# Kernel tuning notes

Hardware: AMD Instinct MI355X
Metric: run time of the kernel (lower is better)

## Reference

```python
import jax, jax.numpy as jnp
import numpy as np

N_EMB = 1024
N_HEADS = 16


def setup_inputs() -> dict:
    key = jax.random.key(0)
    k1, k2, k3 = jax.random.split(key, 3)
    x = jax.random.normal(k1, (2, 2048, N_EMB), dtype=jnp.float32)
    # qkv linear params (torch Linear: y = x @ W.T + b; store W as [in, 3*in])
    W_qkv = jax.random.normal(k2, (N_EMB, 3 * N_EMB), dtype=jnp.float32) * (1.0 / np.sqrt(N_EMB))
    b_qkv = jax.random.normal(k3, (3 * N_EMB,), dtype=jnp.float32) * 0.02
    return {"x": x, "W_qkv": W_qkv, "b_qkv": b_qkv}


def reference(x, W_qkv, b_qkv):
    B, S, D = x.shape
    H = N_HEADS
    Dh = D // H
    qkv = x @ W_qkv + b_qkv                       # [B, S, 3D]
    q, k, v = jnp.split(qkv, 3, axis=-1)
    # [B, S, D] -> [B, H, S, Dh]
    q = q.reshape(B, S, H, Dh).transpose(0, 2, 1, 3)
    k = k.reshape(B, S, H, Dh).transpose(0, 2, 1, 3)
    v = v.reshape(B, S, H, Dh).transpose(0, 2, 1, 3)
    scores = jnp.einsum("bhqd,bhkd->bhqk", q, k) * (1.0 / np.sqrt(Dh))
    attn = jax.nn.softmax(scores, axis=-1)        # no causal mask in original
    out = jnp.einsum("bhqk,bhkd->bhqd", attn, v)  # [B, H, S, Dh]
    return out.transpose(0, 2, 1, 3).reshape(B, S, D)
```

## Files before the change

kernel.cpp:

```cpp
#include <hip/hip_runtime.h>

#define S_LEN 2048
#define D_EMB 1024
#define H_CNT 16
#define DHD   64
#define N_QKV 3072

typedef __attribute__((ext_vector_type(8))) short short8;
typedef __attribute__((ext_vector_type(4))) float f32x4;
typedef unsigned short u16;

__device__ __forceinline__ u16 f2bf(float f) {
  unsigned u = __float_as_uint(f);
  u += 0x7FFFu + ((u >> 16) & 1u);
  return (u16)(u >> 16);
}

__device__ __forceinline__ unsigned cvtpk(float lo, float hi) {
  unsigned r;
  asm("v_cvt_pk_bf16_f32 %0, %1, %2" : "=v"(r) : "v"(lo), "v"(hi));
  return r;
}

__device__ __forceinline__ void gload16(const void* g, void* lds) {
  __builtin_amdgcn_global_load_lds(
      (const __attribute__((address_space(1))) void*)g,
      (__attribute__((address_space(3))) void*)lds, 16, 0, 0);
}

__global__ __launch_bounds__(256) void cvt_x_kern(const float* __restrict__ x,
                                                  u16* __restrict__ xb) {
  int i = blockIdx.x * 256 + threadIdx.x;
  float4 v = ((const float4*)x)[i];
  unsigned* o = (unsigned*)&((ushort4*)xb)[i];
  o[0] = cvtpk(v.x, v.y);
  o[1] = cvtpk(v.z, v.w);
}

__global__ __launch_bounds__(256) void cvt_wt_kern(const float* __restrict__ w,
                                                   u16* __restrict__ wt) {
  __shared__ u16 tile[64][65];
  const int ct = blockIdx.x, kt = blockIdx.y, t = threadIdx.x;
#pragma unroll
  for (int i = 0; i < 4; ++i) {
    int idx = t + i * 256;
    int kk = idx >> 4, c4 = (idx & 15) * 4;
    float4 v = *(const float4*)(w + (size_t)(kt * 64 + kk) * N_QKV + ct * 64 + c4);
    tile[kk][c4 + 0] = f2bf(v.x);
    tile[kk][c4 + 1] = f2bf(v.y);
    tile[kk][c4 + 2] = f2bf(v.z);
    tile[kk][c4 + 3] = f2bf(v.w);
  }
  __syncthreads();
#pragma unroll
  for (int i = 0; i < 2; ++i) {
    int id = t + i * 256;
    int c = id >> 3, k8 = (id & 7) * 8;
    short8 o;
#pragma unroll
    for (int j = 0; j < 8; ++j) o[j] = (short)tile[k8 + j][c];
    *(short8*)&wt[(size_t)(ct * 64 + c) * D_EMB + kt * 64 + k8] = o;
  }
}

__global__ __launch_bounds__(256) void qkv_gemm_kern(
    const u16* __restrict__ xb, const u16* __restrict__ wt,
    const float* __restrict__ bias,
    u16* __restrict__ qo, u16* __restrict__ ko, u16* __restrict__ vo) {
  __shared__ __align__(16) u16 SM[128 * 128];
  u16* As = SM;
  u16* Bs = SM + 128 * 64;
  const int t = threadIdx.x;
  const int w = t >> 6, l = t & 63, lr = l & 15, lg = l >> 4;
  const int wr = w >> 1, wc = w & 1;
  const int row0 = blockIdx.x * 128, col0 = blockIdx.y * 128;
  const int srow = l >> 3, scol = (l & 7) * 16;
  const int tsel = col0 >> 10;
  const bool ctq = (tsel < 2);

  f32x4 acc[4][4];
#pragma unroll
  for (int m = 0; m < 4; ++m)
#pragma unroll
    for (int n = 0; n < 4; ++n) acc[m][n] = (f32x4){0.f, 0.f, 0.f, 0.f};

  const int ldrow = w * 32;
  for (int ki = 0; ki < 16; ++ki) {
    int k0 = ki * 64;
#pragma unroll
    for (int c = 0; c < 4; ++c) {
      int tr = ldrow + c * 8 + srow;
      int sc = scol ^ ((tr & 7) << 4);
      gload16((const char*)xb + (size_t)(row0 + tr) * (D_EMB * 2) + k0 * 2 + sc,
              (char*)As + (ldrow + c * 8) * 128);
      gload16((const char*)wt + (size_t)(col0 + tr) * (D_EMB * 2) + k0 * 2 + sc,
              (char*)Bs + (ldrow + c * 8) * 128);
    }
    __syncthreads();
    const u16* Ab = ctq ? Bs : As;
    const u16* Bb = ctq ? As : Bs;
    const int ar0 = ctq ? wc * 64 : wr * 64;
    const int br0 = ctq ? wr * 64 : wc * 64;
    short8 bfr[4][2];
#pragma unroll
    for (int n = 0; n < 4; ++n) {
      int br = br0 + n * 16 + lr;
#pragma unroll
      for (int kk = 0; kk < 2; ++kk)
        bfr[n][kk] = *(const short8*)&Bb[(br << 6) + ((kk * 32 + lg * 8) ^ ((br & 7) << 3))];
    }
#pragma unroll
    for (int m = 0; m < 4; ++m) {
      int ar = ar0 + m * 16 + lr;
      short8 a0 = *(const short8*)&Ab[(ar << 6) + ((lg * 8) ^ ((ar & 7) << 3))];
      short8 a1 = *(const short8*)&Ab[(ar << 6) + ((32 + lg * 8) ^ ((ar & 7) << 3))];
#pragma unroll
      for (int n = 0; n < 4; ++n) {
        acc[m][n] = __builtin_amdgcn_mfma_f32_16x16x32_bf16(a0, bfr[n][0], acc[m][n], 0, 0, 0);
        acc[m][n] = __builtin_amdgcn_mfma_f32_16x16x32_bf16(a1, bfr[n][1], acc[m][n], 0, 0, 0);
      }
    }
    __syncthreads();
  }

  const int bb = row0 >> 11;
  if (ctq) {
    const float scl = (tsel == 0) ? (0.125f * 1.44269504f) : 1.0f;
    u16* dst = (tsel == 0) ? qo : ko;
#pragma unroll
    for (int m = 0; m < 4; ++m) {
      int qc0 = wc * 64 + m * 16 + lg * 4;
      float4 bn = *(const float4*)&bias[col0 + qc0];
#pragma unroll
      for (int n = 0; n < 4; ++n) {
        int s = wr * 64 + n * 16 + lr;
        uint2 pk;
        pk.x = cvtpk((acc[m][n][0] + bn.x) * scl, (acc[m][n][1] + bn.y) * scl);
        pk.y = cvtpk((acc[m][n][2] + bn.z) * scl, (acc[m][n][3] + bn.w) * scl);
        *(uint2*)&SM[(s << 7) + (qc0 ^ ((s & 7) << 3))] = pk;
      }
    }
    __syncthreads();
    const int c = t & 15, rl = t >> 4;
#pragma unroll
    for (int pass = 0; pass < 8; ++pass) {
      int s = pass * 16 + rl;
      short8 v = *(const short8*)&SM[(s << 7) + ((c ^ (s & 7)) << 3)];
      int d = (col0 + c * 8) & 1023, hh = d >> 6, dh = d & 63;
      *(short8*)(dst + ((size_t)(bb * H_CNT + hh) * S_LEN + (row0 & 2047) + s) * DHD + dh) = v;
    }
  } else {
#pragma unroll
    for (int n = 0; n < 4; ++n) {
      int qc = wc * 64 + n * 16 + lr;
      float bn = bias[col0 + qc];
#pragma unroll
      for (int m = 0; m < 4; ++m) {
        int s0l = wr * 64 + m * 16 + lg * 4;
        uint2 pk;
        pk.x = cvtpk(acc[m][n][0] + bn, acc[m][n][1] + bn);
        pk.y = cvtpk(acc[m][n][2] + bn, acc[m][n][3] + bn);
        *(uint2*)&SM[(qc << 7) + (s0l ^ ((qc & 7) << 3))] = pk;
      }
    }
    __syncthreads();
    const int c = t & 15, rl = t >> 4;
#pragma unroll
    for (int pass = 0; pass < 8; ++pass) {
      int qc = pass * 16 + rl;
      short8 v = *(const short8*)&SM[(qc << 7) + ((c ^ (qc & 7)) << 3)];
      int d = (col0 + qc) & 1023, hh = d >> 6, dh = d & 63;
      *(short8*)(vo + ((size_t)(bb * H_CNT + hh) * DHD + dh) * S_LEN +
                 (row0 & 2047) + c * 8) = v;
    }
  }
}

__global__ __launch_bounds__(256) void attn_kern(
    const u16* __restrict__ qp, const u16* __restrict__ kp,
    const u16* __restrict__ vtp, float* __restrict__ out) {
  __shared__ __align__(16) u16 Ks[2][64 * 64];
  __shared__ __align__(16) u16 Vs[2][64 * 64];
  __shared__ __align__(16) u16 Ps[4][16 * 64];
  const int t = threadIdx.x;
  const int w = t >> 6, l = t & 63, lr = l & 15, lg = l >> 4;
  const int qt = blockIdx.x, bh = blockIdx.y;
  const int b = bh >> 4, h = bh & 15;
  const int srow = l >> 3, scol = (l & 7) * 16;

  const u16* qbase = qp + ((size_t)bh * S_LEN + qt * 64 + w * 16) * DHD;
  short8 qf[2];
#pragma unroll
  for (int kk = 0; kk < 2; ++kk)
    qf[kk] = *(const short8*)(qbase + lr * DHD + kk * 32 + lg * 8);

  float mrun = -__builtin_inff(), lsum = 0.f;
  f32x4 oacc[4];
#pragma unroll
  for (int ct = 0; ct < 4; ++ct) oacc[ct] = (f32x4){0.f, 0.f, 0.f, 0.f};

  const char* kt_g = (const char*)(kp + (size_t)bh * S_LEN * DHD);
  const char* vt_g = (const char*)(vtp + (size_t)bh * DHD * S_LEN);

#define ATTN_STAGE(it, buf)                                                     \
  {                                                                             \
    int kv0 = (it) * 64;                                                        \
    _Pragma("unroll") for (int c = 0; c < 2; ++c) {                             \
      int r8 = w * 16 + c * 8;                                                  \
      int row = r8 + srow;                                                      \
      int sc = scol ^ ((row & 7) << 4);                                         \
      gload16(kt_g + (size_t)(kv0 + row) * 128 + sc, (char*)Ks[buf] + r8 * 128);\
      gload16(vt_g + (size_t)row * (S_LEN * 2) + kv0 * 2 + sc,                  \
              (char*)Vs[buf] + r8 * 128);                                       \
    }                                                                           \
  }

  ATTN_STAGE(0, 0)
  __syncthreads();

  for (int it = 0; it < S_LEN / 64; ++it) {
    int cur = it & 1;
    if (it < S_LEN / 64 - 1) ATTN_STAGE(it + 1, cur ^ 1)

    f32x4 st[4];
#pragma unroll
    for (int k2 = 0; k2 < 4; ++k2) st[k2] = (f32x4){0.f, 0.f, 0.f, 0.f};
#pragma unroll
    for (int kk = 0; kk < 2; ++kk)
#pragma unroll
      for (int k2 = 0; k2 < 4; ++k2) {
        int ar = k2 * 16 + lr;
        short8 a = *(const short8*)&Ks[cur][(ar << 6) +
                                           ((kk * 32 + lg * 8) ^ ((ar & 7) << 3))];
        st[k2] = __builtin_amdgcn_mfma_f32_16x16x32_bf16(a, qf[kk], st[k2], 0, 0, 0);
      }

    float mx = -__builtin_inff();
#pragma unroll
    for (int k2 = 0; k2 < 4; ++k2)
#pragma unroll
      for (int r = 0; r < 4; ++r) mx = fmaxf(mx, st[k2][r]);
    mx = fmaxf(mx, __shfl_xor(mx, 16, 64));
    mx = fmaxf(mx, __shfl_xor(mx, 32, 64));
    if (!__all(mx - mrun <= 8.0f)) {
      float mnew = fmaxf(mrun, mx);
      float fsc = exp2f(mrun - mnew);
      float fr[4];
#pragma unroll
      for (int r = 0; r < 4; ++r) fr[r] = __shfl(fsc, lg * 4 + r, 64);
#pragma unroll
      for (int ct = 0; ct < 4; ++ct)
#pragma unroll
        for (int r = 0; r < 4; ++r) oacc[ct][r] *= fr[r];
      lsum *= fsc;
      mrun = mnew;
    }
    float rs = 0.f;
#pragma unroll
    for (int k2 = 0; k2 < 4; ++k2) {
      float p0 = exp2f(st[k2][0] - mrun), p1 = exp2f(st[k2][1] - mrun);
      float p2 = exp2f(st[k2][2] - mrun), p3 = exp2f(st[k2][3] - mrun);
      rs += (p0 + p1) + (p2 + p3);
      int key0 = k2 * 16 + lg * 4;
      int e = key0 ^ ((lr & 7) << 3);
      *(unsigned*)&Ps[w][(lr << 6) + e + 0] = cvtpk(p0, p1);
      *(unsigned*)&Ps[w][(lr << 6) + e + 2] = cvtpk(p2, p3);
    }
    rs += __shfl_xor(rs, 16, 64);
    rs += __shfl_xor(rs, 32, 64);
    lsum += rs;

    short8 pa[2];
#pragma unroll
    for (int kk = 0; kk < 2; ++kk)
      pa[kk] = *(const short8*)&Ps[w][(lr << 6) + ((kk * 32 + lg * 8) ^ ((lr & 7) << 3))];
#pragma unroll
    for (int ct = 0; ct < 4; ++ct)
#pragma unroll
      for (int kk = 0; kk < 2; ++kk) {
        int br = ct * 16 + lr;
        short8 bv = *(const short8*)&Vs[cur][(br << 6) +
                                            ((kk * 32 + lg * 8) ^ ((br & 7) << 3))];
        oacc[ct] = __builtin_amdgcn_mfma_f32_16x16x32_bf16(pa[kk], bv, oacc[ct], 0, 0, 0);
      }
    __syncthreads();
  }

  float inv = 1.0f / lsum;
  float invr[4];
#pragma unroll
  for (int r = 0; r < 4; ++r) invr[r] = __shfl(inv, lg * 4 + r, 64);
  const int qg0 = qt * 64 + w * 16 + lg * 4;
#pragma unroll
  for (int ct = 0; ct < 4; ++ct) {
    int col = h * 64 + ct * 16 + lr;
#pragma unroll
    for (int r = 0; r < 4; ++r)
      out[((size_t)b * S_LEN + qg0 + r) * D_EMB + col] = oacc[ct][r] * invr[r];
  }
}

extern "C" void kernel_launch(void* const* d_in, const int* in_sizes, int n_in,
                              void* d_out, int out_size, void* d_ws, size_t ws_size,
                              hipStream_t stream) {
  (void)in_sizes; (void)n_in; (void)out_size; (void)ws_size;
  const float* x  = (const float*)d_in[0];
  const float* Wq = (const float*)d_in[1];
  const float* bq = (const float*)d_in[2];
  float* out = (float*)d_out;
  char* ws = (char*)d_ws;
  u16* xb = (u16*)(ws);
  u16* wt = (u16*)(ws + (size_t)8  * 1024 * 1024);
  u16* qb = (u16*)(ws + (size_t)14 * 1024 * 1024);
  u16* kb = (u16*)(ws + (size_t)22 * 1024 * 1024);
  u16* vb = (u16*)(ws + (size_t)30 * 1024 * 1024);

  cvt_x_kern <<<4096, 256, 0, stream>>>(x, xb);
  cvt_wt_kern<<<dim3(48, 16), 256, 0, stream>>>(Wq, wt);
  qkv_gemm_kern<<<dim3(32, 24), 256, 0, stream>>>(xb, wt, bq, qb, kb, vb);
  attn_kern  <<<dim3(32, 32), 256, 0, stream>>>(qb, kb, vb, out);
}
```

Measured before the change: 196.5 us.

## Keep P in registers by permuting K rows at load time, drop LDS P round-trip

The probability tile is no longer written to and re-read from shared memory. K rows are instead loaded into LDS in a permuted order (tau mapping), so the MFMA score output layout already matches the A-operand layout needed for the PV MFMA, and P is packed straight from registers into bf16. The KV loop is also unrolled by two with compile-time buffer indices and pointer-increment addressing. This removes LDS writes and reads plus the associated latency per tile, but relies on the permutation being correct for the key/value pairing, since the softmax sum is order-independent while V must use the same key order.

Result: faster. 190.4 us (-3.1%).

```diff
diff --git a/kernel.cpp b/kernel.cpp
--- a/kernel.cpp
+++ b/kernel.cpp
@@ -8,6 +8,7 @@
 
 typedef __attribute__((ext_vector_type(8))) short short8;
 typedef __attribute__((ext_vector_type(4))) float f32x4;
+typedef __attribute__((ext_vector_type(4))) unsigned u32x4;
 typedef unsigned short u16;
 
 __device__ __forceinline__ u16 f2bf(float f) {
@@ -181,7 +182,6 @@
     const u16* __restrict__ vtp, float* __restrict__ out) {
   __shared__ __align__(16) u16 Ks[2][64 * 64];
   __shared__ __align__(16) u16 Vs[2][64 * 64];
-  __shared__ __align__(16) u16 Ps[4][16 * 64];
   const int t = threadIdx.x;
   const int w = t >> 6, l = t & 63, lr = l & 15, lg = l >> 4;
   const int qt = blockIdx.x, bh = blockIdx.y;
@@ -199,91 +199,92 @@
 #pragma unroll
   for (int ct = 0; ct < 4; ++ct) oacc[ct] = (f32x4){0.f, 0.f, 0.f, 0.f};
 
-  const char* kt_g = (const char*)(kp + (size_t)bh * S_LEN * DHD);
-  const char* vt_g = (const char*)(vtp + (size_t)bh * DHD * S_LEN);
-
-#define ATTN_STAGE(it, buf)                                                     \
-  {                                                                             \
-    int kv0 = (it) * 64;                                                        \
-    _Pragma("unroll") for (int c = 0; c < 2; ++c) {                             \
-      int r8 = w * 16 + c * 8;                                                  \
-      int row = r8 + srow;                                                      \
-      int sc = scol ^ ((row & 7) << 4);                                         \
-      gload16(kt_g + (size_t)(kv0 + row) * 128 + sc, (char*)Ks[buf] + r8 * 128);\
-      gload16(vt_g + (size_t)row * (S_LEN * 2) + kv0 * 2 + sc,                  \
-              (char*)Vs[buf] + r8 * 128);                                       \
-    }                                                                           \
-  }
-
-  ATTN_STAGE(0, 0)
+  int koff[2], voff[2];
+#pragma unroll
+  for (int c = 0; c < 2; ++c) {
+    int row = w * 16 + c * 8 + srow;
+    int sc = scol ^ ((row & 7) << 4);
+    int tau = ((row & 15) >> 2) * 8 + ((row >> 4) & 1) * 4 + (row & 3) + (row >> 5) * 32;
+    koff[c] = tau * 128 + sc;
+    voff[c] = row * (S_LEN * 2) + sc;
+  }
+  const char* kpt = (const char*)(kp + (size_t)bh * S_LEN * DHD);
+  const char* vpt = (const char*)(vtp + (size_t)bh * DHD * S_LEN);
+
+#define ATTN_STAGE(BUF)                                                   \
+  {                                                                       \
+    _Pragma("unroll") for (int c = 0; c < 2; ++c) {                       \
+      int r8 = w * 16 + c * 8;                                            \
+      gload16(kpt + koff[c], (char*)Ks[BUF] + r8 * 128);                  \
+      gload16(vpt + voff[c], (char*)Vs[BUF] + r8 * 128);                  \
+    }                                                                     \
+    kpt += 64 * 128;                                                      \
+    vpt += 64 * 2;                                                        \
+  }
+
+#define ATTN_TILE(BUF, PF)                                                        \
+  {                                                                               \
+    if (PF) ATTN_STAGE(BUF ^ 1)                                                   \
+    f32x4 st[4];                                                                  \
+    _Pragma("unroll") for (int k2 = 0; k2 < 4; ++k2)                              \
+        st[k2] = (f32x4){0.f, 0.f, 0.f, 0.f};                                     \
+    _Pragma("unroll") for (int kk = 0; kk < 2; ++kk)                              \
+      _Pragma("unroll") for (int k2 = 0; k2 < 4; ++k2) {                          \
+        int ar = k2 * 16 + lr;                                                    \
+        short8 a = *(const short8*)&Ks[BUF][(ar << 6) +                           \
+                                            ((kk * 32 + lg * 8) ^ ((ar & 7) << 3))]; \
+        st[k2] = __builtin_amdgcn_mfma_f32_16x16x32_bf16(a, qf[kk], st[k2], 0, 0, 0); \
+      }                                                                           \
+    float mx = fmaxf(fmaxf(fmaxf(st[0][0], st[0][1]), fmaxf(st[0][2], st[0][3])), \
+                     fmaxf(fmaxf(st[1][0], st[1][1]), fmaxf(st[1][2], st[1][3]))); \
+    mx = fmaxf(mx, fmaxf(fmaxf(fmaxf(st[2][0], st[2][1]), fmaxf(st[2][2], st[2][3])), \
+                         fmaxf(fmaxf(st[3][0], st[3][1]), fmaxf(st[3][2], st[3][3])))); \
+    mx = fmaxf(mx, __shfl_xor(mx, 16, 64));                                       \
+    mx = fmaxf(mx, __shfl_xor(mx, 32, 64));                                       \
+    if (!__all(mx - mrun <= 8.0f)) {                                              \
+      float mnew = fmaxf(mrun, mx);                                               \
+      float fsc = exp2f(mrun - mnew);                                             \
+      float fr[4];                                                                \
+      _Pragma("unroll") for (int r = 0; r < 4; ++r)                               \
+          fr[r] = __shfl(fsc, lg * 4 + r, 64);                                    \
+      _Pragma("unroll") for (int ct = 0; ct < 4; ++ct)                            \
+        _Pragma("unroll") for (int r = 0; r < 4; ++r) oacc[ct][r] *= fr[r];       \
+      lsum *= fsc;                                                                \
+      mrun = mnew;                                                                \
+    }                                                                             \
+    float rs = 0.f;                                                               \
+    _Pragma("unroll") for (int k2 = 0; k2 < 4; ++k2)                              \
+      _Pragma("unroll") for (int r = 0; r < 4; ++r) {                             \
+        st[k2][r] = exp2f(st[k2][r] - mrun);                                      \
+        rs += st[k2][r];                                                          \
+      }                                                                           \
+    rs += __shfl_xor(rs, 16, 64);                                                 \
+    rs += __shfl_xor(rs, 32, 64);                                                 \
+    lsum += rs;                                                                   \
+    u32x4 ua, ub;                                                                 \
+    ua[0] = cvtpk(st[0][0], st[0][1]); ua[1] = cvtpk(st[0][2], st[0][3]);         \
+    ua[2] = cvtpk(st[1][0], st[1][1]); ua[3] = cvtpk(st[1][2], st[1][3]);         \
+    ub[0] = cvtpk(st[2][0], st[2][1]); ub[1] = cvtpk(st[2][2], st[2][3]);         \
+    ub[2] = cvtpk(st[3][0], st[3][1]); ub[3] = cvtpk(st[3][2], st[3][3]);         \
+    short8 pa0 = __builtin_bit_cast(short8, ua);                                  \
+    short8 pa1 = __builtin_bit_cast(short8, ub);                                  \
+    _Pragma("unroll") for (int ct = 0; ct < 4; ++ct) {                            \
+      int br = ct * 16 + lr;                                                      \
+      short8 bv0 = *(const short8*)&Vs[BUF][(br << 6) +                           \
+                                            ((lg * 8) ^ ((br & 7) << 3))];        \
+      short8 bv1 = *(const short8*)&Vs[BUF][(br << 6) +                           \
+                                            ((32 + lg * 8) ^ ((br & 7) << 3))];   \
+      oacc[ct] = __builtin_amdgcn_mfma_f32_16x16x32_bf16(pa0, bv0, oacc[ct], 0, 0, 0); \
+      oacc[ct] = __builtin_amdgcn_mfma_f32_16x16x32_bf16(pa1, bv1, oacc[ct], 0, 0, 0); \
+    }                                                                             \
+    __syncthreads();                                                              \
+  }
+
+  ATTN_STAGE(0)
   __syncthreads();
-
-  for (int it = 0; it < S_LEN / 64; ++it) {
-    int cur = it & 1;
-    if (it < S_LEN / 64 - 1) ATTN_STAGE(it + 1, cur ^ 1)
-
-    f32x4 st[4];
-#pragma unroll
-    for (int k2 = 0; k2 < 4; ++k2) st[k2] = (f32x4){0.f, 0.f, 0.f, 0.f};
-#pragma unroll
-    for (int kk = 0; kk < 2; ++kk)
-#pragma unroll
-      for (int k2 = 0; k2 < 4; ++k2) {
-        int ar = k2 * 16 + lr;
-        short8 a = *(const short8*)&Ks[cur][(ar << 6) +
-                                           ((kk * 32 + lg * 8) ^ ((ar & 7) << 3))];
-        st[k2] = __builtin_amdgcn_mfma_f32_16x16x32_bf16(a, qf[kk], st[k2], 0, 0, 0);
-      }
-
-    float mx = -__builtin_inff();
-#pragma unroll
-    for (int k2 = 0; k2 < 4; ++k2)
-#pragma unroll
-      for (int r = 0; r < 4; ++r) mx = fmaxf(mx, st[k2][r]);
-    mx = fmaxf(mx, __shfl_xor(mx, 16, 64));
-    mx = fmaxf(mx, __shfl_xor(mx, 32, 64));
-    if (!__all(mx - mrun <= 8.0f)) {
-      float mnew = fmaxf(mrun, mx);
-      float fsc = exp2f(mrun - mnew);
-      float fr[4];
-#pragma unroll
-      for (int r = 0; r < 4; ++r) fr[r] = __shfl(fsc, lg * 4 + r, 64);
-#pragma unroll
-      for (int ct = 0; ct < 4; ++ct)
-#pragma unroll
-        for (int r = 0; r < 4; ++r) oacc[ct][r] *= fr[r];
-      lsum *= fsc;
-      mrun = mnew;
-    }
-    float rs = 0.f;
-#pragma unroll
-    for (int k2 = 0; k2 < 4; ++k2) {
-      float p0 = exp2f(st[k2][0] - mrun), p1 = exp2f(st[k2][1] - mrun);
-      float p2 = exp2f(st[k2][2] - mrun), p3 = exp2f(st[k2][3] - mrun);
-      rs += (p0 + p1) + (p2 + p3);
-      int key0 = k2 * 16 + lg * 4;
-      int e = key0 ^ ((lr & 7) << 3);
-      *(unsigned*)&Ps[w][(lr << 6) + e + 0] = cvtpk(p0, p1);
-      *(unsigned*)&Ps[w][(lr << 6) + e + 2] = cvtpk(p2, p3);
-    }
-    rs += __shfl_xor(rs, 16, 64);
-    rs += __shfl_xor(rs, 32, 64);
-    lsum += rs;
-
-    short8 pa[2];
-#pragma unroll
-    for (int kk = 0; kk < 2; ++kk)
-      pa[kk] = *(const short8*)&Ps[w][(lr << 6) + ((kk * 32 + lg * 8) ^ ((lr & 7) << 3))];
-#pragma unroll
-    for (int ct = 0; ct < 4; ++ct)
-#pragma unroll
-      for (int kk = 0; kk < 2; ++kk) {
-        int br = ct * 16 + lr;
-        short8 bv = *(const short8*)&Vs[cur][(br << 6) +
-                                            ((kk * 32 + lg * 8) ^ ((br & 7) << 3))];
-        oacc[ct] = __builtin_amdgcn_mfma_f32_16x16x32_bf16(pa[kk], bv, oacc[ct], 0, 0, 0);
-      }
-    __syncthreads();
+  for (int ii = 0; ii < 16; ++ii) {
+    ATTN_TILE(0, 1)
+    ATTN_TILE(1, ii < 15)
   }
 
   float inv = 1.0f / lsum;
```

## Load K/V fragments straight to registers and keep P in registers

Applied to the files above, without the earlier changes.

The attention kernel drops the shared-memory double buffer for K and V and the per-wave P scratch. Each wave now loads its own K and V MFMA fragments directly from global memory into registers, prefetching the next tile while the current one is computed. The key order is permuted so the softmax probabilities can be packed straight into MFMA A operands without an LDS round trip, and s_setprio is raised around the MFMA blocks. This removes LDS traffic and block-wide barriers. In exchange, each of the four waves re-reads the same K/V tiles from global memory or cache, and register pressure rises.

Measured after the change: 347.2 us. 1.77x slower.

```diff
diff --git a/kernel.cpp b/kernel.cpp
--- a/kernel.cpp
+++ b/kernel.cpp
@@ -8,6 +8,7 @@
 
 typedef __attribute__((ext_vector_type(8))) short short8;
 typedef __attribute__((ext_vector_type(4))) float f32x4;
+typedef __attribute__((ext_vector_type(4))) unsigned u32x4;
 typedef unsigned short u16;
 
 __device__ __forceinline__ u16 f2bf(float f) {
@@ -179,67 +180,68 @@
 __global__ __launch_bounds__(256) void attn_kern(
     const u16* __restrict__ qp, const u16* __restrict__ kp,
     const u16* __restrict__ vtp, float* __restrict__ out) {
-  __shared__ __align__(16) u16 Ks[2][64 * 64];
-  __shared__ __align__(16) u16 Vs[2][64 * 64];
-  __shared__ __align__(16) u16 Ps[4][16 * 64];
   const int t = threadIdx.x;
   const int w = t >> 6, l = t & 63, lr = l & 15, lg = l >> 4;
   const int qt = blockIdx.x, bh = blockIdx.y;
   const int b = bh >> 4, h = bh & 15;
-  const int srow = l >> 3, scol = (l & 7) * 16;
 
   const u16* qbase = qp + ((size_t)bh * S_LEN + qt * 64 + w * 16) * DHD;
-  short8 qf[2];
-#pragma unroll
-  for (int kk = 0; kk < 2; ++kk)
-    qf[kk] = *(const short8*)(qbase + lr * DHD + kk * 32 + lg * 8);
+  short8 qf0 = *(const short8*)(qbase + lr * DHD + lg * 8);
+  short8 qf1 = *(const short8*)(qbase + lr * DHD + 32 + lg * 8);
 
   float mrun = -__builtin_inff(), lsum = 0.f;
   f32x4 oacc[4];
 #pragma unroll
   for (int ct = 0; ct < 4; ++ct) oacc[ct] = (f32x4){0.f, 0.f, 0.f, 0.f};
 
-  const char* kt_g = (const char*)(kp + (size_t)bh * S_LEN * DHD);
-  const char* vt_g = (const char*)(vtp + (size_t)bh * DHD * S_LEN);
-
-#define ATTN_STAGE(it, buf)                                                     \
-  {                                                                             \
-    int kv0 = (it) * 64;                                                        \
-    _Pragma("unroll") for (int c = 0; c < 2; ++c) {                             \
-      int r8 = w * 16 + c * 8;                                                  \
-      int row = r8 + srow;                                                      \
-      int sc = scol ^ ((row & 7) << 4);                                         \
-      gload16(kt_g + (size_t)(kv0 + row) * 128 + sc, (char*)Ks[buf] + r8 * 128);\
-      gload16(vt_g + (size_t)row * (S_LEN * 2) + kv0 * 2 + sc,                  \
-              (char*)Vs[buf] + r8 * 128);                                       \
-    }                                                                           \
-  }
-
-  ATTN_STAGE(0, 0)
-  __syncthreads();
-
-  for (int it = 0; it < S_LEN / 64; ++it) {
-    int cur = it & 1;
-    if (it < S_LEN / 64 - 1) ATTN_STAGE(it + 1, cur ^ 1)
-
+  const int key0 = (lr >> 2) * 8 + (lr & 3);
+  const u16* kpA = kp + (size_t)bh * S_LEN * DHD + (size_t)key0 * DHD + lg * 8;
+  const u16* kpB = kpA + 32 * DHD;
+  const u16* vp0 = vtp + (size_t)bh * DHD * S_LEN + (size_t)lr * S_LEN + lg * 8;
+  const u16* vp1 = vp0 + 16 * S_LEN;
+  const u16* vp2 = vp0 + 32 * S_LEN;
+  const u16* vp3 = vp0 + 48 * S_LEN;
+
+  short8 kf[4][2], vf[4][2];
+#pragma unroll
+  for (int kk = 0; kk < 2; ++kk) {
+    kf[0][kk] = *(const short8*)(kpA + kk * 32);
+    kf[1][kk] = *(const short8*)(kpA + 4 * DHD + kk * 32);
+    kf[2][kk] = *(const short8*)(kpB + kk * 32);
+    kf[3][kk] = *(const short8*)(kpB + 4 * DHD + kk * 32);
+    vf[0][kk] = *(const short8*)(vp0 + kk * 32);
+    vf[1][kk] = *(const short8*)(vp1 + kk * 32);
+    vf[2][kk] = *(const short8*)(vp2 + kk * 32);
+    vf[3][kk] = *(const short8*)(vp3 + kk * 32);
+  }
+
+  for (int it = 0; it < 32; ++it) {
     f32x4 st[4];
 #pragma unroll
     for (int k2 = 0; k2 < 4; ++k2) st[k2] = (f32x4){0.f, 0.f, 0.f, 0.f};
-#pragma unroll
-    for (int kk = 0; kk < 2; ++kk)
-#pragma unroll
-      for (int k2 = 0; k2 < 4; ++k2) {
-        int ar = k2 * 16 + lr;
-        short8 a = *(const short8*)&Ks[cur][(ar << 6) +
-                                           ((kk * 32 + lg * 8) ^ ((ar & 7) << 3))];
-        st[k2] = __builtin_amdgcn_mfma_f32_16x16x32_bf16(a, qf[kk], st[k2], 0, 0, 0);
-      }
-
-    float mx = -__builtin_inff();
-#pragma unroll
-    for (int k2 = 0; k2 < 4; ++k2)
-#pragma unroll
-      for (int r = 0; r < 4; ++r) mx = fmaxf(mx, st[k2][r]);
+    __builtin_amdgcn_s_setprio(1);
+#pragma unroll
+    for (int k2 = 0; k2 < 4; ++k2) {
+      st[k2] = __builtin_amdgcn_mfma_f32_16x16x32_bf16(kf[k2][0], qf0, st[k2], 0, 0, 0);
+      st[k2] = __builtin_amdgcn_mfma_f32_16x16x32_bf16(kf[k2][1], qf1, st[k2], 0, 0, 0);
+    }
+    __builtin_amdgcn_s_setprio(0);
+
+    int kstep = (it == 31) ? 0 : 64 * DHD;
+    kpA += kstep;
+    kpB += kstep;
+#pragma unroll
+    for (int kk = 0; kk < 2; ++kk) {
+      kf[0][kk] = *(const short8*)(kpA + kk * 32);
+      kf[1][kk] = *(const short8*)(kpA + 4 * DHD + kk * 32);
+      kf[2][kk] = *(const short8*)(kpB + kk * 32);
+      kf[3][kk] = *(const short8*)(kpB + 4 * DHD + kk * 32);
+    }
+
+    float mx = fmaxf(fmaxf(fmaxf(st[0][0], st[0][1]), fmaxf(st[0][2], st[0][3])),
+                     fmaxf(fmaxf(st[1][0], st[1][1]), fmaxf(st[1][2], st[1][3])));
+    mx = fmaxf(mx, fmaxf(fmaxf(fmaxf(st[2][0], st[2][1]), fmaxf(st[2][2], st[2][3])),
+                         fmaxf(fmaxf(st[3][0], st[3][1]), fmaxf(st[3][2], st[3][3]))));
     mx = fmaxf(mx, __shfl_xor(mx, 16, 64));
     mx = fmaxf(mx, __shfl_xor(mx, 32, 64));
     if (!__all(mx - mrun <= 8.0f)) {
@@ -257,33 +259,40 @@
     }
     float rs = 0.f;
 #pragma unroll
-    for (int k2 = 0; k2 < 4; ++k2) {
-      float p0 = exp2f(st[k2][0] - mrun), p1 = exp2f(st[k2][1] - mrun);
-      float p2 = exp2f(st[k2][2] - mrun), p3 = exp2f(st[k2][3] - mrun);
-      rs += (p0 + p1) + (p2 + p3);
-      int key0 = k2 * 16 + lg * 4;
-      int e = key0 ^ ((lr & 7) << 3);
-      *(unsigned*)&Ps[w][(lr << 6) + e + 0] = cvtpk(p0, p1);
-      *(unsigned*)&Ps[w][(lr << 6) + e + 2] = cvtpk(p2, p3);
-    }
+    for (int k2 = 0; k2 < 4; ++k2)
+#pragma unroll
+      for (int r = 0; r < 4; ++r) {
+        st[k2][r] = exp2f(st[k2][r] - mrun);
+        rs += st[k2][r];
+      }
     rs += __shfl_xor(rs, 16, 64);
     rs += __shfl_xor(rs, 32, 64);
     lsum += rs;
-
-    short8 pa[2];
-#pragma unroll
-    for (int kk = 0; kk < 2; ++kk)
-      pa[kk] = *(const short8*)&Ps[w][(lr << 6) + ((kk * 32 + lg * 8) ^ ((lr & 7) << 3))];
-#pragma unroll
-    for (int ct = 0; ct < 4; ++ct)
-#pragma unroll
-      for (int kk = 0; kk < 2; ++kk) {
-        int br = ct * 16 + lr;
-        short8 bv = *(const short8*)&Vs[cur][(br << 6) +
-                                            ((kk * 32 + lg * 8) ^ ((br & 7) << 3))];
-        oacc[ct] = __builtin_amdgcn_mfma_f32_16x16x32_bf16(pa[kk], bv, oacc[ct], 0, 0, 0);
-      }
-    __syncthreads();
+    u32x4 ua, ub;
+    ua[0] = cvtpk(st[0][0], st[0][1]); ua[1] = cvtpk(st[0][2], st[0][3]);
+    ua[2] = cvtpk(st[1][0], st[1][1]); ua[3] = cvtpk(st[1][2], st[1][3]);
+    ub[0] = cvtpk(st[2][0], st[2][1]); ub[1] = cvtpk(st[2][2], st[2][3]);
+    ub[2] = cvtpk(st[3][0], st[3][1]); ub[3] = cvtpk(st[3][2], st[3][3]);
+    short8 pa0 = __builtin_bit_cast(short8, ua);
+    short8 pa1 = __builtin_bit_cast(short8, ub);
+
+    __builtin_amdgcn_s_setprio(1);
+#pragma unroll
+    for (int ct = 0; ct < 4; ++ct) {
+      oacc[ct] = __builtin_amdgcn_mfma_f32_16x16x32_bf16(pa0, vf[ct][0], oacc[ct], 0, 0, 0);
+      oacc[ct] = __builtin_amdgcn_mfma_f32_16x16x32_bf16(pa1, vf[ct][1], oacc[ct], 0, 0, 0);
+    }
+    __builtin_amdgcn_s_setprio(0);
+
+    int vstep = (it == 31) ? 0 : 64;
+    vp0 += vstep; vp1 += vstep; vp2 += vstep; vp3 += vstep;
+#pragma unroll
+    for (int kk = 0; kk < 2; ++kk) {
+      vf[0][kk] = *(const short8*)(vp0 + kk * 32);
+      vf[1][kk] = *(const short8*)(vp1 + kk * 32);
+      vf[2][kk] = *(const short8*)(vp2 + kk * 32);
+      vf[3][kk] = *(const short8*)(vp3 + kk * 32);
+    }
   }
 
   float inv = 1.0f / lsum;
```
